# Kernel optimization log

Hardware: AMD Instinct MI355X
Metric: run time of the kernel (lower is better)

Reference implementation:

```python
import jax, jax.numpy as jnp
import numpy as np

VOCAB, D_MODEL, HEADS, PAD_ID = 32000, 512, 8, 0
D_K = D_MODEL // HEADS
EPS = 1e-5


def pos_encoding(T, d):
    pos = jnp.arange(T, dtype=jnp.float32)[:, None]              # [T,1]
    freqs = 1.0 / (10000.0 ** (jnp.arange(0, d, 2, dtype=jnp.float32) / d))
    ang = pos * freqs                                            # [T,d/2]
    pe = jnp.zeros((T, d), dtype=jnp.float32)
    pe = pe.at[:, 0::2].set(jnp.sin(ang)).at[:, 1::2].set(jnp.cos(ang))
    return pe


def layer_norm(x, g, b):
    mu = jnp.mean(x, axis=-1, keepdims=True)
    var = jnp.var(x, axis=-1, keepdims=True)
    return (x - mu) * jax.lax.rsqrt(var + EPS) * g + b


def setup_inputs() -> dict:
    key = jax.random.key(0)
    ks = jax.random.split(key, 12)
    B, T = 4, 2048
    s = 0.02
    inp = {
        "tokens": jax.random.randint(ks[0], (B, T), 0, VOCAB),
        "emb": jax.random.normal(ks[1], (VOCAB, D_MODEL), jnp.float32) * s,
        "wq": jax.random.normal(ks[2], (D_MODEL, D_MODEL), jnp.float32) * s,
        "bq": jnp.zeros((D_MODEL,), jnp.float32),
        "wk": jax.random.normal(ks[3], (D_MODEL, D_MODEL), jnp.float32) * s,
        "bk": jnp.zeros((D_MODEL,), jnp.float32),
        "wv": jax.random.normal(ks[4], (D_MODEL, D_MODEL), jnp.float32) * s,
        "bv": jnp.zeros((D_MODEL,), jnp.float32),
        "wo": jax.random.normal(ks[5], (D_MODEL, D_MODEL), jnp.float32) * s,
        "bo": jnp.zeros((D_MODEL,), jnp.float32),
        "w1": jax.random.normal(ks[6], (D_MODEL, 2 * D_MODEL), jnp.float32) * s,
        "b1": jnp.zeros((2 * D_MODEL,), jnp.float32),
        "w2": jax.random.normal(ks[7], (2 * D_MODEL, D_MODEL), jnp.float32) * s,
        "b2": jnp.zeros((D_MODEL,), jnp.float32),
        "ln1_g": jnp.ones((D_MODEL,), jnp.float32),
        "ln1_b": jnp.zeros((D_MODEL,), jnp.float32),
        "ln2_g": jnp.ones((D_MODEL,), jnp.float32),
        "ln2_b": jnp.zeros((D_MODEL,), jnp.float32),
    }
    return inp


def reference(tokens, emb, wq, bq, wk, bk, wv, bv, wo, bo,
              w1, b1, w2, b2, ln1_g, ln1_b, ln2_g, ln2_b):
    B, T = tokens.shape
    x = emb[tokens] * jnp.sqrt(jnp.float32(D_MODEL))             # [B,T,D]
    x = x + pos_encoding(T, D_MODEL)[None]                       # add PE
    q = (x @ wq + bq).reshape(B, T, HEADS, D_K)
    k = (x @ wk + bk).reshape(B, T, HEADS, D_K)
    v = (x @ wv + bv).reshape(B, T, HEADS, D_K)
    scores = jnp.einsum("bqhd,bkhd->bhqk", q, k) / jnp.sqrt(jnp.float32(D_K))
    key_pad_mask = tokens == PAD_ID                              # [B,T]
    neg = jnp.finfo(scores.dtype).min
    scores = jnp.where(key_pad_mask[:, None, None, :], neg, scores)
    attn = jax.nn.softmax(scores, axis=-1)                       # [B,H,T,T]
    av = jnp.einsum("bhqk,bkhd->bqhd", attn, v).reshape(B, T, D_MODEL)
    av = av @ wo + bo
    h = layer_norm(av + x, ln1_g, ln1_b)
    ff = jax.nn.relu(h @ w1 + b1) @ w2 + b2
    out = layer_norm(h + ff, ln2_g, ln2_b)
    return out, key_pad_mask
```

## Files before the change

kernel.cpp:

```cpp
#include <hip/hip_runtime.h>
#include <hip/hip_bf16.h>
#include <math.h>

#define D_MODEL 512
#define HEADS   8
#define D_K     64
#define T_SEQ   2048
#define B_SZ    4
#define NROWS   (B_SZ * T_SEQ)
#define KVB     64
#define KSPLIT  2
#define KHALF   (T_SEQ / KSPLIT)

#define BM 128
#define BN 128
#define BKG 64

typedef __attribute__((ext_vector_type(8))) short short8;
typedef __attribute__((ext_vector_type(4))) float f32x4;
typedef __attribute__((ext_vector_type(4))) ushort bf16x4;
typedef __attribute__((ext_vector_type(4))) unsigned int u32x4;

typedef __attribute__((address_space(1))) const unsigned int as1_uint;
typedef __attribute__((address_space(3))) unsigned int as3_uint;

__device__ __forceinline__ ushort f2bf(float f) {
    union { float f; unsigned u; } v; v.f = f;
    unsigned u = v.u;
    unsigned r = (u + 0x7FFFu + ((u >> 16) & 1u)) >> 16;
    return (ushort)r;
}
__device__ __forceinline__ float bf2f(ushort u) {
    union { unsigned u; float f; } v; v.u = ((unsigned)u) << 16;
    return v.f;
}
__device__ __forceinline__ unsigned pk_bf16(float lo, float hi) {
    unsigned r;
    asm("v_cvt_pk_bf16_f32 %0, %1, %2" : "=v"(r) : "v"(lo), "v"(hi));
    return r;
}

__global__ __launch_bounds__(256) void k_prep(
    const int* __restrict__ tokens, const float* __restrict__ emb,
    const float* __restrict__ wq, const float* __restrict__ wk,
    const float* __restrict__ wv, const float* __restrict__ wo,
    const float* __restrict__ w1, const float* __restrict__ w2,
    const float* __restrict__ bq, const float* __restrict__ bk,
    const float* __restrict__ bv,
    ushort* __restrict__ xb, float* __restrict__ mask_out,
    ushort* __restrict__ wqkvT, ushort* __restrict__ woT,
    ushort* __restrict__ w1T, ushort* __restrict__ w2T,
    float* __restrict__ bqkv, float qsc)
{
    __shared__ ushort tls[32][33];
    int bid = blockIdx.x, tid = threadIdx.x;
    if (bid < 4096) {
        int row = bid * 2 + (tid >> 7);
        int t   = row & (T_SEQ - 1);
        int tok = tokens[row];
        int t2  = tid & 127;
        if (t2 == 0) mask_out[row] = (tok == 0) ? 1.0f : 0.0f;
        const float* e = emb + (size_t)tok * D_MODEL;
#pragma unroll
        for (int i = 0; i < 4; ++i) {
            int d = t2 + 128 * i;
            float freq = exp2f(-(float)(d & ~1) * 0.025952563240330564f);
            float sn, cs;
            sincosf((float)t * freq, &sn, &cs);
            float x = e[d] * 22.627416997969522f + ((d & 1) ? cs : sn);
            xb[(size_t)row * D_MODEL + d] = f2bf(x);
        }
        return;
    }
    const float* src; ushort* dst; float scale = 1.0f; int K, N, bx, by;
    if (bid < 5120) {
        int b = bid - 4096; int z = b >> 8; int rem = b & 255;
        bx = rem & 15; by = rem >> 4; K = 512; N = 512;
        src = (z == 0) ? wq : (z == 1) ? wk : (z == 2) ? wv : wo;
        dst = (z < 3) ? wqkvT + (size_t)z * 512 * 512 : woT;
        scale = (z == 0) ? qsc : 1.0f;
    } else if (bid < 5632) {
        int b = bid - 5120; bx = b & 31; by = b >> 5; K = 512; N = 1024; src = w1; dst = w1T;
    } else if (bid < 6144) {
        int b = bid - 5632; bx = b & 15; by = b >> 4; K = 1024; N = 512; src = w2; dst = w2T;
    } else {
        int i = (bid - 6144) * 256 + tid;
        if (i < 512)       bqkv[i] = bq[i] * qsc;
        else if (i < 1024) bqkv[i] = bk[i - 512];
        else if (i < 1536) bqkv[i] = bv[i - 1024];
        return;
    }
    int tx = tid & 31, ty = tid >> 5;
    int n0 = bx * 32, k0 = by * 32;
#pragma unroll
    for (int i = 0; i < 4; ++i)
        tls[ty + i * 8][tx] = f2bf(src[(size_t)(k0 + ty + i * 8) * N + n0 + tx] * scale);
    __syncthreads();
#pragma unroll
    for (int i = 0; i < 4; ++i)
        dst[(size_t)(n0 + ty + i * 8) * K + k0 + tx] = tls[tx][ty + i * 8];
}

template<int MODE, bool RELU>
__global__ __launch_bounds__(256) void k_gemm_lds(
    const ushort* __restrict__ A, const ushort* __restrict__ BT,
    const float* __restrict__ bias, void* __restrict__ C0,
    void* __restrict__ C1, void* __restrict__ C2,
    int M, int N, int K)
{
    __shared__ __attribute__((aligned(16))) ushort As[2][BM * BKG];
    __shared__ __attribute__((aligned(16))) ushort Bs[2][BN * BKG];

    const int tid = threadIdx.x;
    const int w = tid >> 6, l = tid & 63;
    const int lr = l & 15, lg = l >> 4;
    const int wr = w >> 1, wc = w & 1;

    int bx = blockIdx.x, by = blockIdx.y;
    {
        int nx = gridDim.x, ny = gridDim.y;
        if ((ny & 7) == 0) {
            int lin = bx + nx * by;
            int xcd = lin & 7, idx = lin >> 3;
            int per = ny >> 3;
            by = xcd * per + (idx % per);
            bx = idx / per;
        }
    }
    const int brow0 = by * BM;
    const int bcol0 = bx * BN;
    const int gi0 = w * 256 + l;
    const int swz = lr & 7;

    f32x4 acc[4][4] = {};
    const int nks = K >> 6;

#define STAGE(buf, k0)                                                          \
    {                                                                           \
        _Pragma("unroll")                                                       \
        for (int i = 0; i < 4; ++i) {                                           \
            int gi = gi0 + i * 64;                                              \
            int row = gi >> 3, slot = gi & 7;                                   \
            int g = slot ^ (row & 7);                                           \
            __builtin_amdgcn_global_load_lds(                                   \
                (as1_uint*)(A + (size_t)(brow0 + row) * K + (k0) + g * 8),      \
                (as3_uint*)(&As[buf][gi * 8]), 16, 0, 0);                       \
            __builtin_amdgcn_global_load_lds(                                   \
                (as1_uint*)(BT + (size_t)(bcol0 + row) * K + (k0) + g * 8),     \
                (as3_uint*)(&Bs[buf][gi * 8]), 16, 0, 0);                       \
        }                                                                       \
    }

    STAGE(0, 0);
    __syncthreads();

    int buf = 0;
    for (int ks = 0; ks < nks; ++ks) {
        if (ks + 1 < nks) STAGE(buf ^ 1, (ks + 1) * BKG);
#pragma unroll
        for (int kk = 0; kk < 2; ++kk) {
            short8 af[4], bfr[4];
#pragma unroll
            for (int m = 0; m < 4; ++m) {
                int row = wr * 64 + m * 16 + lr;
                int slot = (kk * 4 + lg) ^ swz;
                af[m] = *(const short8*)(&As[buf][row * 64 + slot * 8]);
            }
#pragma unroll
            for (int n = 0; n < 4; ++n) {
                int row = wc * 64 + n * 16 + lr;
                int slot = (kk * 4 + lg) ^ swz;
                bfr[n] = *(const short8*)(&Bs[buf][row * 64 + slot * 8]);
            }
#pragma unroll
            for (int m = 0; m < 4; ++m)
#pragma unroll
                for (int n = 0; n < 4; ++n)
                    acc[m][n] = __builtin_amdgcn_mfma_f32_16x16x32_bf16(af[m], bfr[n], acc[m][n], 0, 0, 0);
        }
        __syncthreads();
        buf ^= 1;
    }
#undef STAGE

#pragma unroll
    for (int n = 0; n < 4; ++n) {
        int col = bcol0 + wc * 64 + n * 16 + lr;
        float bv = bias[col];
#pragma unroll
        for (int m = 0; m < 4; ++m) {
            int row0 = brow0 + wr * 64 + m * 16 + 4 * lg;
            if constexpr (MODE == 2) {
                int seg = col >> 9, lc = col & 511;
                if (seg == 2) {
                    bf16x4 pk;
#pragma unroll
                    for (int j = 0; j < 4; ++j) pk[j] = f2bf(acc[m][n][j] + bv);
                    *(bf16x4*)((ushort*)C2 + (size_t)lc * M + row0) = pk;
                } else {
                    ushort* dst = (seg == 0) ? (ushort*)C0 : (ushort*)C1;
#pragma unroll
                    for (int j = 0; j < 4; ++j)
                        dst[(size_t)(row0 + j) * 512 + lc] = f2bf(acc[m][n][j] + bv);
                }
            } else if constexpr (MODE == 0) {
#pragma unroll
                for (int j = 0; j < 4; ++j) {
                    float v = acc[m][n][j] + bv;
                    if (RELU) v = fmaxf(v, 0.0f);
                    ((ushort*)C0)[(size_t)(row0 + j) * N + col] = f2bf(v);
                }
            } else {
#pragma unroll
                for (int j = 0; j < 4; ++j)
                    ((float*)C0)[(size_t)(row0 + j) * N + col] = acc[m][n][j] + bv;
            }
        }
    }
}

__global__ __launch_bounds__(512, 4) void k_attn(
    const ushort* __restrict__ Q, const ushort* __restrict__ Kb,
    const ushort* __restrict__ Vt, const int* __restrict__ tokens,
    ushort* __restrict__ O0, ushort* __restrict__ O1,
    float* __restrict__ lp)
{
    __shared__ __attribute__((aligned(16))) ushort Kl[2][KVB * 64];
    __shared__ __attribute__((aligned(16))) ushort Vl[2][KVB * 64];
    __shared__ __attribute__((aligned(16))) ushort Mbh[KHALF];
    __shared__ int padf[KHALF / KVB];

    const int tid = threadIdx.x;
    const int w = tid >> 6, l = tid & 63;
    const int lr = l & 15, lg = l >> 4;
    const int swz = lr & 7;

    int lin = blockIdx.x + 8 * (blockIdx.y + 8 * blockIdx.z);
    int xcd = lin & 7, idx = lin >> 3;
    int qt  = idx & 7;
    int grp = xcd + 8 * (idx >> 3);
    int ks  = grp & 1;
    int h   = (grp >> 1) & 7;
    int b   = grp >> 4;

    const int q0  = qt * 256 + w * 32;
    const int kb0 = ks * KHALF;

    const int gi   = w * 64 + l;
    const int srow = gi >> 3;
    const int sg   = gi & 7;
    const int sgx  = sg ^ (srow & 7);
    const ushort* Ksrc = Kb + ((size_t)(b * T_SEQ + kb0) + srow) * D_MODEL + h * D_K + sgx * 8;
    const int kbase = 32 * (sg >> 2) + 8 * ((sg >> 1) & 1) + 4 * (sg & 1);
    const ushort* Vsrc = Vt + (size_t)(h * D_K + srow) * NROWS + b * T_SEQ + kb0 + kbase;
    const int vds = srow * 128 + sgx * 16;

#define KSTAGE(bufi, kt_)                                                       \
    __builtin_amdgcn_global_load_lds(                                           \
        (as1_uint*)(Ksrc + (size_t)(kt_) * KVB * D_MODEL),                      \
        (as3_uint*)(&Kl[bufi][gi * 8]), 16, 0, 0);

    const ushort* Qh = Q + (size_t)b * T_SEQ * D_MODEL + h * D_K;
    short8 aq[2][2];
#pragma unroll
    for (int qs = 0; qs < 2; ++qs)
#pragma unroll
        for (int c2 = 0; c2 < 2; ++c2)
            aq[qs][c2] = *(const short8*)(Qh + (size_t)(q0 + qs * 16 + lr) * D_MODEL
                                          + c2 * 32 + 8 * lg);

    const int* tk = tokens + b * T_SEQ + kb0;
#pragma unroll
    for (int it = 0; it < KHALF / 512; ++it) {
        int i = tid + it * 512;
        bool pad = (tk[i] == 0);
        Mbh[i] = pad ? (ushort)0xFF7F : (ushort)0;
        unsigned long long bal = __ballot(pad);
        if (l == 0) padf[it * 8 + w] = (bal != 0ull);
    }

    float l_run[2] = {0.0f, 0.0f};
    f32x4 acc[2][4] = {};

    {
        bf16x4 va = *(const bf16x4*)(Vsrc);
        bf16x4 vb2 = *(const bf16x4*)(Vsrc + 16);
        KSTAGE(0, 0);
        u32x4 pk = { ((const unsigned*)&va)[0], ((const unsigned*)&va)[1],
                     ((const unsigned*)&vb2)[0], ((const unsigned*)&vb2)[1] };
        *(u32x4*)((char*)Vl[0] + vds) = pk;
    }
    __syncthreads();

    int buf = 0;
    const int NT = KHALF / KVB;
    for (int kt = 0; kt < NT; ++kt) {
        bf16x4 vna, vnb;
        bool more = (kt + 1 < NT);
        if (more) {
            KSTAGE(buf ^ 1, kt + 1);
            vna = *(const bf16x4*)(Vsrc + (kt + 1) * KVB);
            vnb = *(const bf16x4*)(Vsrc + (kt + 1) * KVB + 16);
        }

        const ushort* Kt = Kl[buf];
        const ushort* Vb = Vl[buf];
        bool havePad = padf[kt];

        unsigned dw[2][4][2];
#pragma unroll
        for (int kh = 0; kh < 2; ++kh) {
            short8 kf[2][2];
#pragma unroll
            for (int i = 0; i < 2; ++i)
#pragma unroll
                for (int c2 = 0; c2 < 2; ++c2)
                    kf[i][c2] = *(const short8*)((const char*)Kt
                                + ((2 * kh + i) * 16 + lr) * 128
                                + (((c2 * 4 + lg) ^ swz) * 16));
#pragma unroll
            for (int qs = 0; qs < 2; ++qs)
#pragma unroll
                for (int i = 0; i < 2; ++i) {
                    int kb = 2 * kh + i;
                    __builtin_amdgcn_s_setprio(1);
                    f32x4 sf = {};
                    sf = __builtin_amdgcn_mfma_f32_16x16x32_bf16(kf[i][0], aq[qs][0], sf, 0, 0, 0);
                    sf = __builtin_amdgcn_mfma_f32_16x16x32_bf16(kf[i][1], aq[qs][1], sf, 0, 0, 0);
                    __builtin_amdgcn_s_setprio(0);
                    if (havePad) {
                        bf16x4 m4 = *(const bf16x4*)(Mbh + kt * KVB + kb * 16 + 4 * lg);
#pragma unroll
                        for (int j = 0; j < 4; ++j) sf[j] += bf2f(m4[j]);
                    }
                    float p0 = exp2f(sf[0]);
                    float p1 = exp2f(sf[1]);
                    float p2 = exp2f(sf[2]);
                    float p3 = exp2f(sf[3]);
                    l_run[qs] += (p0 + p1) + (p2 + p3);
                    dw[qs][kb][0] = pk_bf16(p0, p1);
                    dw[qs][kb][1] = pk_bf16(p2, p3);
                }
        }

#pragma unroll
        for (int ch = 0; ch < 2; ++ch) {
            short8 vf[2][2];
#pragma unroll
            for (int i = 0; i < 2; ++i)
#pragma unroll
                for (int kk = 0; kk < 2; ++kk)
                    vf[i][kk] = *(const short8*)((const char*)Vb
                                + ((2 * ch + i) * 16 + lr) * 128
                                + (((kk * 4 + lg) ^ swz) * 16));
            __builtin_amdgcn_s_setprio(1);
#pragma unroll
            for (int qs = 0; qs < 2; ++qs) {
                u32x4 pw0 = { dw[qs][0][0], dw[qs][0][1], dw[qs][1][0], dw[qs][1][1] };
                u32x4 pw1 = { dw[qs][2][0], dw[qs][2][1], dw[qs][3][0], dw[qs][3][1] };
                short8 pa0 = __builtin_bit_cast(short8, pw0);
                short8 pa1 = __builtin_bit_cast(short8, pw1);
#pragma unroll
                for (int i = 0; i < 2; ++i) {
                    int c = 2 * ch + i;
                    acc[qs][c] = __builtin_amdgcn_mfma_f32_16x16x32_bf16(vf[i][0], pa0, acc[qs][c], 0, 0, 0);
                    acc[qs][c] = __builtin_amdgcn_mfma_f32_16x16x32_bf16(vf[i][1], pa1, acc[qs][c], 0, 0, 0);
                }
            }
            __builtin_amdgcn_s_setprio(0);
        }

        if (more) {
            u32x4 pk = { ((const unsigned*)&vna)[0], ((const unsigned*)&vna)[1],
                         ((const unsigned*)&vnb)[0], ((const unsigned*)&vnb)[1] };
            *(u32x4*)((char*)Vl[buf ^ 1] + vds) = pk;
        }
        __syncthreads();
        buf ^= 1;
    }
#undef KSTAGE

    ushort* Op = (ks == 0) ? O0 : O1;
#pragma unroll
    for (int qs = 0; qs < 2; ++qs) {
        ushort* orow = Op + (size_t)(b * T_SEQ + q0 + qs * 16 + lr) * D_MODEL + h * D_K;
#pragma unroll
        for (int c = 0; c < 4; ++c) {
            bf16x4 pk;
#pragma unroll
            for (int j = 0; j < 4; ++j) pk[j] = f2bf(acc[qs][c][j]);
            *(bf16x4*)(orow + c * 16 + 4 * lg) = pk;
        }
        float ls = l_run[qs];
        ls += __shfl_xor(ls, 16);
        ls += __shfl_xor(ls, 32);
        if (l < 16)
            lp[(size_t)(ks * 8 + h) * NROWS + b * T_SEQ + q0 + qs * 16 + l] = ls;
    }
}

__global__ __launch_bounds__(256) void k_comb(
    ushort* __restrict__ O0, const ushort* __restrict__ O1,
    const float* __restrict__ lp)
{
    int g = blockIdx.x * 256 + threadIdx.x;
    int row = g >> 6, seg = g & 63;
    int h = seg >> 3;
    size_t off = (size_t)row * D_MODEL + seg * 8;
    short8 a = *(const short8*)(O0 + off);
    short8 c = *(const short8*)(O1 + off);
    float l0 = lp[(size_t)h * NROWS + row];
    float l1 = lp[(size_t)(8 + h) * NROWS + row];
    float rl = 1.0f / (l0 + l1);
    short8 r;
#pragma unroll
    for (int i = 0; i < 8; ++i)
        r[i] = (short)f2bf((bf2f((ushort)a[i]) + bf2f((ushort)c[i])) * rl);
    *(short8*)(O0 + off) = r;
}

template<bool A_BF16, bool RES_BF16, bool OUT_F32>
__global__ __launch_bounds__(256) void k_ln(
    const void* __restrict__ A, const void* __restrict__ Res,
    const float* __restrict__ g, const float* __restrict__ bb,
    float* __restrict__ of, ushort* __restrict__ ob)
{
    int row = blockIdx.x * 4 + (threadIdx.x >> 6);
    int l = threadIdx.x & 63;
    float v[8];
    float s = 0.0f, ss = 0.0f;
#pragma unroll
    for (int i = 0; i < 2; ++i) {
        int d0 = i * 256 + l * 4;
        f32x4 va, vb;
        if (A_BF16) {
            bf16x4 t = *(const bf16x4*)((const ushort*)A + (size_t)row * D_MODEL + d0);
#pragma unroll
            for (int j = 0; j < 4; ++j) va[j] = bf2f(t[j]);
        } else {
            va = *(const f32x4*)((const float*)A + (size_t)row * D_MODEL + d0);
        }
        if (RES_BF16) {
            bf16x4 t = *(const bf16x4*)((const ushort*)Res + (size_t)row * D_MODEL + d0);
#pragma unroll
            for (int j = 0; j < 4; ++j) vb[j] = bf2f(t[j]);
        } else {
            vb = *(const f32x4*)((const float*)Res + (size_t)row * D_MODEL + d0);
        }
#pragma unroll
        for (int j = 0; j < 4; ++j) {
            float x = va[j] + vb[j];
            v[i * 4 + j] = x; s += x; ss += x * x;
        }
    }
#pragma unroll
    for (int d = 1; d < 64; d <<= 1) { s += __shfl_xor(s, d); ss += __shfl_xor(ss, d); }
    float mu  = s * (1.0f / 512.0f);
    float var = ss * (1.0f / 512.0f) - mu * mu;
    float rs  = rsqrtf(var + 1e-5f);
#pragma unroll
    for (int i = 0; i < 2; ++i)
#pragma unroll
        for (int j = 0; j < 4; ++j) {
            int d = i * 256 + l * 4 + j;
            float o = (v[i * 4 + j] - mu) * rs * g[d] + bb[d];
            if (OUT_F32) of[(size_t)row * D_MODEL + d] = o;
            else         ob[(size_t)row * D_MODEL + d] = f2bf(o);
        }
}

extern "C" void kernel_launch(void* const* d_in, const int* in_sizes, int n_in,
                              void* d_out, int out_size, void* d_ws, size_t ws_size,
                              hipStream_t stream)
{
    const int*   tokens = (const int*)  d_in[0];
    const float* emb    = (const float*)d_in[1];
    const float* wq     = (const float*)d_in[2];
    const float* bq     = (const float*)d_in[3];
    const float* wk     = (const float*)d_in[4];
    const float* bk     = (const float*)d_in[5];
    const float* wv     = (const float*)d_in[6];
    const float* bv     = (const float*)d_in[7];
    const float* wo     = (const float*)d_in[8];
    const float* bo     = (const float*)d_in[9];
    const float* w1     = (const float*)d_in[10];
    const float* b1     = (const float*)d_in[11];
    const float* w2     = (const float*)d_in[12];
    const float* b2     = (const float*)d_in[13];
    const float* ln1_g  = (const float*)d_in[14];
    const float* ln1_b  = (const float*)d_in[15];
    const float* ln2_g  = (const float*)d_in[16];
    const float* ln2_b  = (const float*)d_in[17];

    char* ws = (char*)d_ws;
    ushort* xb   = (ushort*)(ws + 0);
    ushort* Qb   = (ushort*)(ws + 8388608);
    ushort* Kbuf = (ushort*)(ws + 16777216);
    ushort* Vt   = (ushort*)(ws + 25165824);
    ushort* atb  = (ushort*)(ws + 33554432);
    ushort* AVb  = (ushort*)(ws + 41943040);
    ushort* wqkvT = (ushort*)(ws + 50331648);
    ushort* woT  = wqkvT + 1536 * 512;
    ushort* w1T  = woT + 262144;
    ushort* w2T  = w1T + 524288;
    float*  bqkv = (float*)(w2T + 524288);
    float*  lpart = bqkv + 2048;

    ushort* hb   = Qb;
    ushort* ff1b = Kbuf;
    ushort* ff2b = AVb;

    float* out_f    = (float*)d_out;
    float* mask_out = out_f + (size_t)NROWS * D_MODEL;

    const float QSC = 0.18033688011112042f;

    k_prep<<<6150, 256, 0, stream>>>(
        tokens, emb, wq, wk, wv, wo, w1, w2, bq, bk, bv,
        xb, mask_out, wqkvT, woT, w1T, w2T, bqkv, QSC);

    k_gemm_lds<2, false><<<dim3(12, 64), 256, 0, stream>>>(
        xb, wqkvT, bqkv, Qb, Kbuf, Vt, NROWS, 1536, 512);

    k_attn<<<dim3(8, 8, 8), 512, 0, stream>>>(
        Qb, Kbuf, Vt, tokens, atb, AVb, lpart);
    k_comb<<<2048, 256, 0, stream>>>(atb, AVb, lpart);

    k_gemm_lds<0, false><<<dim3(4, 64), 256, 0, stream>>>(
        atb, woT, bo, AVb, nullptr, nullptr, NROWS, 512, 512);

    k_ln<true, true, false><<<NROWS / 4, 256, 0, stream>>>(
        AVb, xb, ln1_g, ln1_b, nullptr, hb);

    k_gemm_lds<0, true><<<dim3(8, 64), 256, 0, stream>>>(
        hb, w1T, b1, ff1b, nullptr, nullptr, NROWS, 1024, 512);
    k_gemm_lds<0, false><<<dim3(4, 64), 256, 0, stream>>>(
        ff1b, w2T, b2, ff2b, nullptr, nullptr, NROWS, 512, 1024);

    k_ln<true, true, true><<<NROWS / 4, 256, 0, stream>>>(
        ff2b, hb, ln2_g, ln2_b, out_f, nullptr);
}
```

Before: 166.1 us.

## Template GEMM row tile, use 64-row tiles for small GEMMs, MFMA row-sum in attention

Makes the GEMM row-tile height a template parameter and launches the output-projection and both FFN GEMMs with 64-row tiles, doubling their grid size so more workgroups cover the 256 CUs. In attention, the per-row softmax denominator is now accumulated by an extra MFMA against a vector of bf16 ones instead of scalar adds plus cross-lane shuffles. This moves VALU work onto the matrix units, at the cost of extra MFMAs and summing bf16-rounded probabilities rather than fp32 values. Smaller GEMM tiles also lower per-workgroup data reuse.

```diff
diff --git a/kernel.cpp b/kernel.cpp
--- a/kernel.cpp
+++ b/kernel.cpp
@@ -12,7 +12,6 @@
 #define KSPLIT  2
 #define KHALF   (T_SEQ / KSPLIT)
 
-#define BM 128
 #define BN 128
 #define BKG 64
 
@@ -101,14 +100,15 @@
         dst[(size_t)(n0 + ty + i * 8) * K + k0 + tx] = tls[tx][ty + i * 8];
 }
 
-template<int MODE, bool RELU>
+template<int MODE, bool RELU, int BMT>
 __global__ __launch_bounds__(256) void k_gemm_lds(
     const ushort* __restrict__ A, const ushort* __restrict__ BT,
     const float* __restrict__ bias, void* __restrict__ C0,
     void* __restrict__ C1, void* __restrict__ C2,
     int M, int N, int K)
 {
-    __shared__ __attribute__((aligned(16))) ushort As[2][BM * BKG];
+    constexpr int MR = BMT / 32;
+    __shared__ __attribute__((aligned(16))) ushort As[2][BMT * BKG];
     __shared__ __attribute__((aligned(16))) ushort Bs[2][BN * BKG];
 
     const int tid = threadIdx.x;
@@ -127,24 +127,29 @@
             bx = idx / per;
         }
     }
-    const int brow0 = by * BM;
+    const int brow0 = by * BMT;
     const int bcol0 = bx * BN;
-    const int gi0 = w * 256 + l;
-    const int swz = lr & 7;
-
-    f32x4 acc[4][4] = {};
+    const int swz = lr & 15 & 7;
+
+    f32x4 acc[MR][4] = {};
     const int nks = K >> 6;
 
 #define STAGE(buf, k0)                                                          \
     {                                                                           \
         _Pragma("unroll")                                                       \
-        for (int i = 0; i < 4; ++i) {                                           \
-            int gi = gi0 + i * 64;                                              \
+        for (int i = 0; i < BMT / 32; ++i) {                                    \
+            int gi = w * (BMT * 2) + i * 64 + l;                                \
             int row = gi >> 3, slot = gi & 7;                                   \
             int g = slot ^ (row & 7);                                           \
             __builtin_amdgcn_global_load_lds(                                   \
                 (as1_uint*)(A + (size_t)(brow0 + row) * K + (k0) + g * 8),      \
                 (as3_uint*)(&As[buf][gi * 8]), 16, 0, 0);                       \
+        }                                                                       \
+        _Pragma("unroll")                                                       \
+        for (int i = 0; i < 4; ++i) {                                           \
+            int gi = w * 256 + i * 64 + l;                                      \
+            int row = gi >> 3, slot = gi & 7;                                   \
+            int g = slot ^ (row & 7);                                           \
             __builtin_amdgcn_global_load_lds(                                   \
                 (as1_uint*)(BT + (size_t)(bcol0 + row) * K + (k0) + g * 8),     \
                 (as3_uint*)(&Bs[buf][gi * 8]), 16, 0, 0);                       \
@@ -159,10 +164,10 @@
         if (ks + 1 < nks) STAGE(buf ^ 1, (ks + 1) * BKG);
 #pragma unroll
         for (int kk = 0; kk < 2; ++kk) {
-            short8 af[4], bfr[4];
-#pragma unroll
-            for (int m = 0; m < 4; ++m) {
-                int row = wr * 64 + m * 16 + lr;
+            short8 af[MR], bfr[4];
+#pragma unroll
+            for (int m = 0; m < MR; ++m) {
+                int row = wr * (BMT / 2) + m * 16 + lr;
                 int slot = (kk * 4 + lg) ^ swz;
                 af[m] = *(const short8*)(&As[buf][row * 64 + slot * 8]);
             }
@@ -173,7 +178,7 @@
                 bfr[n] = *(const short8*)(&Bs[buf][row * 64 + slot * 8]);
             }
 #pragma unroll
-            for (int m = 0; m < 4; ++m)
+            for (int m = 0; m < MR; ++m)
 #pragma unroll
                 for (int n = 0; n < 4; ++n)
                     acc[m][n] = __builtin_amdgcn_mfma_f32_16x16x32_bf16(af[m], bfr[n], acc[m][n], 0, 0, 0);
@@ -188,8 +193,8 @@
         int col = bcol0 + wc * 64 + n * 16 + lr;
         float bv = bias[col];
 #pragma unroll
-        for (int m = 0; m < 4; ++m) {
-            int row0 = brow0 + wr * 64 + m * 16 + 4 * lg;
+        for (int m = 0; m < MR; ++m) {
+            int row0 = brow0 + wr * (BMT / 2) + m * 16 + 4 * lg;
             if constexpr (MODE == 2) {
                 int seg = col >> 9, lc = col & 511;
                 if (seg == 2) {
@@ -269,6 +274,10 @@
             aq[qs][c2] = *(const short8*)(Qh + (size_t)(q0 + qs * 16 + lr) * D_MODEL
                                           + c2 * 32 + 8 * lg);
 
+    short8 vones;
+#pragma unroll
+    for (int i = 0; i < 8; ++i) vones[i] = (short)0x3F80;
+
     const int* tk = tokens + b * T_SEQ + kb0;
 #pragma unroll
     for (int it = 0; it < KHALF / 512; ++it) {
@@ -279,8 +288,8 @@
         if (l == 0) padf[it * 8 + w] = (bal != 0ull);
     }
 
-    float l_run[2] = {0.0f, 0.0f};
     f32x4 acc[2][4] = {};
+    f32x4 acc_l[2] = {};
 
     {
         bf16x4 va = *(const bf16x4*)(Vsrc);
@@ -333,13 +342,8 @@
 #pragma unroll
                         for (int j = 0; j < 4; ++j) sf[j] += bf2f(m4[j]);
                     }
-                    float p0 = exp2f(sf[0]);
-                    float p1 = exp2f(sf[1]);
-                    float p2 = exp2f(sf[2]);
-                    float p3 = exp2f(sf[3]);
-                    l_run[qs] += (p0 + p1) + (p2 + p3);
-                    dw[qs][kb][0] = pk_bf16(p0, p1);
-                    dw[qs][kb][1] = pk_bf16(p2, p3);
+                    dw[qs][kb][0] = pk_bf16(exp2f(sf[0]), exp2f(sf[1]));
+                    dw[qs][kb][1] = pk_bf16(exp2f(sf[2]), exp2f(sf[3]));
                 }
         }
 
@@ -366,6 +370,10 @@
                     acc[qs][c] = __builtin_amdgcn_mfma_f32_16x16x32_bf16(vf[i][0], pa0, acc[qs][c], 0, 0, 0);
                     acc[qs][c] = __builtin_amdgcn_mfma_f32_16x16x32_bf16(vf[i][1], pa1, acc[qs][c], 0, 0, 0);
                 }
+                if (ch == 0) {
+                    acc_l[qs] = __builtin_amdgcn_mfma_f32_16x16x32_bf16(vones, pa0, acc_l[qs], 0, 0, 0);
+                    acc_l[qs] = __builtin_amdgcn_mfma_f32_16x16x32_bf16(vones, pa1, acc_l[qs], 0, 0, 0);
+                }
             }
             __builtin_amdgcn_s_setprio(0);
         }
@@ -391,11 +399,8 @@
             for (int j = 0; j < 4; ++j) pk[j] = f2bf(acc[qs][c][j]);
             *(bf16x4*)(orow + c * 16 + 4 * lg) = pk;
         }
-        float ls = l_run[qs];
-        ls += __shfl_xor(ls, 16);
-        ls += __shfl_xor(ls, 32);
         if (l < 16)
-            lp[(size_t)(ks * 8 + h) * NROWS + b * T_SEQ + q0 + qs * 16 + l] = ls;
+            lp[(size_t)(ks * 8 + h) * NROWS + b * T_SEQ + q0 + qs * 16 + l] = acc_l[qs][0];
     }
 }
 
@@ -519,22 +524,22 @@
         tokens, emb, wq, wk, wv, wo, w1, w2, bq, bk, bv,
         xb, mask_out, wqkvT, woT, w1T, w2T, bqkv, QSC);
 
-    k_gemm_lds<2, false><<<dim3(12, 64), 256, 0, stream>>>(
+    k_gemm_lds<2, false, 128><<<dim3(12, 64), 256, 0, stream>>>(
         xb, wqkvT, bqkv, Qb, Kbuf, Vt, NROWS, 1536, 512);
 
     k_attn<<<dim3(8, 8, 8), 512, 0, stream>>>(
         Qb, Kbuf, Vt, tokens, atb, AVb, lpart);
     k_comb<<<2048, 256, 0, stream>>>(atb, AVb, lpart);
 
-    k_gemm_lds<0, false><<<dim3(4, 64), 256, 0, stream>>>(
+    k_gemm_lds<0, false, 64><<<dim3(4, 128), 256, 0, stream>>>(
         atb, woT, bo, AVb, nullptr, nullptr, NROWS, 512, 512);
 
     k_ln<true, true, false><<<NROWS / 4, 256, 0, stream>>>(
         AVb, xb, ln1_g, ln1_b, nullptr, hb);
 
-    k_gemm_lds<0, true><<<dim3(8, 64), 256, 0, stream>>>(
+    k_gemm_lds<0, true, 64><<<dim3(8, 128), 256, 0, stream>>>(
         hb, w1T, b1, ff1b, nullptr, nullptr, NROWS, 1024, 512);
-    k_gemm_lds<0, false><<<dim3(4, 64), 256, 0, stream>>>(
+    k_gemm_lds<0, false, 64><<<dim3(4, 128), 256, 0, stream>>>(
         ff1b, w2T, b2, ff2b, nullptr, nullptr, NROWS, 512, 1024);
 
     k_ln<true, true, true><<<NROWS / 4, 256, 0, stream>>>(
```

After: 156.5 us. -5.8%, faster.
